# Performance work log

Measured on AMD Instinct MI355X. Metric: run time of the kernel, lower is better.

## Reference

```python
import jax, jax.numpy as jnp
import numpy as np

D_MODEL = 1024
EXPAND = 2
D_INNER = D_MODEL * EXPAND  # 2048
D_CONV = 4
B, T = 4, 4096
LN_EPS = 1e-5


def setup_inputs() -> dict:
    key = jax.random.key(0)
    ks = jax.random.split(key, 6)
    x = jax.random.normal(ks[0], (B, T, D_MODEL), dtype=jnp.float32)
    gamma = jnp.ones((D_MODEL,), jnp.float32)
    beta = jnp.zeros((D_MODEL,), jnp.float32)
    # in_proj: Linear(d_model -> 2*d_inner, bias=False); torch weight [out,in]
    W_in = jax.random.normal(ks[1], (2 * D_INNER, D_MODEL), jnp.float32) / np.sqrt(D_MODEL)
    # depthwise conv1d: weight [d_inner, 1, d_conv], bias [d_inner]
    conv_w = jax.random.normal(ks[2], (D_INNER, 1, D_CONV), jnp.float32) / np.sqrt(D_CONV)
    conv_b = jax.random.normal(ks[3], (D_INNER,), jnp.float32) * 0.01
    # out_proj: Linear(d_inner -> d_model, bias=False)
    W_out = jax.random.normal(ks[4], (D_MODEL, D_INNER), jnp.float32) / np.sqrt(D_INNER)
    return {"x": x, "gamma": gamma, "beta": beta, "W_in": W_in,
            "conv_w": conv_w, "conv_b": conv_b, "W_out": W_out}


def _silu(v):
    return v * jax.nn.sigmoid(v)


def reference(x, gamma, beta, W_in, conv_w, conv_b, W_out):
    residual = x
    # LayerNorm
    mu = jnp.mean(x, axis=-1, keepdims=True)
    var = jnp.mean(jnp.square(x - mu), axis=-1, keepdims=True)
    xn = (x - mu) * jax.lax.rsqrt(var + LN_EPS) * gamma + beta
    # in_proj -> split gate
    xz = jnp.einsum('btd,ed->bte', xn, W_in)  # [B,T,2*D_INNER]
    x_part, z = jnp.split(xz, 2, axis=-1)
    # causal depthwise conv: torch pads both sides by d_conv-1 then slices [:T]
    # == left pad (d_conv-1), no right pad
    lhs = jnp.transpose(x_part, (0, 2, 1))  # [B, D_INNER, T]
    x_conv = jax.lax.conv_general_dilated(
        lhs, conv_w, window_strides=(1,), padding=[(D_CONV - 1, 0)],
        feature_group_count=D_INNER,
        dimension_numbers=('NCH', 'OIH', 'NCH')) + conv_b[None, :, None]
    x_conv = jnp.transpose(x_conv, (0, 2, 1))  # [B,T,D_INNER]
    y = _silu(x_conv) * _silu(z)
    out = jnp.einsum('bte,de->btd', y, W_out)
    return residual + out  # dropout=0 (eval) -> identity
```

## Files before the change

### kernel.cpp

```cpp
#include <hip/hip_runtime.h>
#include <hip/hip_bf16.h>

#define D_MODEL 1024
#define D_INNER 2048
#define NTOK    16384
#define TLEN    4096
#define LN_EPS  1e-5f

typedef unsigned short u16;
typedef unsigned short u16x4 __attribute__((ext_vector_type(4)));
typedef unsigned short u16x8 __attribute__((ext_vector_type(8)));
typedef __bf16        bf16x8 __attribute__((ext_vector_type(8)));
typedef float         f32x4  __attribute__((ext_vector_type(4)));

__device__ __forceinline__ float b2f(u16 u) {
    union { float f; unsigned int i; } v; v.i = ((unsigned int)u) << 16; return v.f;
}
__device__ __forceinline__ u16 f2b(float f) {
    union { float f; unsigned int i; } v; v.f = f;
    unsigned int r = v.i + 0x7fffu + ((v.i >> 16) & 1u);
    return (u16)(r >> 16);
}

__device__ __forceinline__ void gld_lds16(const u16* g, u16* l) {
    __builtin_amdgcn_global_load_lds(
        (const __attribute__((address_space(1))) void*)g,
        (__attribute__((address_space(3))) void*)l, 16, 0, 0);
}

__device__ __forceinline__ void ln_body(
    int row, int tid,
    const float* __restrict__ x, const float* __restrict__ gamma,
    const float* __restrict__ beta, u16* __restrict__ xn)
{
    const float* xr = x + (size_t)row * D_MODEL;
    const int c0 = tid * 4;

    f32x4 xv = *(const f32x4*)(xr + c0);
    float s = 0.f, s2 = 0.f;
#pragma unroll
    for (int i = 0; i < 4; i++) { s += xv[i]; s2 += xv[i] * xv[i]; }

#pragma unroll
    for (int off = 32; off > 0; off >>= 1) {
        s  += __shfl_down(s,  off);
        s2 += __shfl_down(s2, off);
    }
    __shared__ float red[8];
    const int wave = tid >> 6, lane = tid & 63;
    if (lane == 0) { red[wave] = s; red[4 + wave] = s2; }
    __syncthreads();
    const float ts  = red[0] + red[1] + red[2] + red[3];
    const float ts2 = red[4] + red[5] + red[6] + red[7];
    const float mu  = ts * (1.0f / D_MODEL);
    const float var = ts2 * (1.0f / D_MODEL) - mu * mu;
    const float inv = rsqrtf(var + LN_EPS);

    f32x4 gv = *(const f32x4*)(gamma + c0);
    f32x4 bv = *(const f32x4*)(beta + c0);
    u16x4 out;
#pragma unroll
    for (int i = 0; i < 4; i++)
        out[i] = f2b((xv[i] - mu) * inv * gv[i] + bv[i]);
    *(u16x4*)(xn + (size_t)row * D_MODEL + c0) = out;
}

__global__ __launch_bounds__(256) void prep_kernel(
    const float* __restrict__ x, const float* __restrict__ gamma,
    const float* __restrict__ beta, u16* __restrict__ xn,
    const float* __restrict__ W_in, u16* __restrict__ wbin,
    const float* __restrict__ W_out, u16* __restrict__ wbout,
    const float* __restrict__ conv_w, float* __restrict__ wt,
    int lnRows)
{
    const int b   = blockIdx.x;
    const int tid = threadIdx.x;

    if (b < lnRows) {
        ln_body(b, tid, x, gamma, beta, xn);
        return;
    }
    int rb = b - lnRows;
    if (rb < 4096) {
        const int o = (rb * 256 + tid) * 4;
        f32x4 v = *(const f32x4*)(W_in + o);
        u16x4 w;
#pragma unroll
        for (int j = 0; j < 4; j++) w[j] = f2b(v[j]);
        *(u16x4*)(wbin + o) = w;
        return;
    }
    rb -= 4096;
    if (rb < 2048) {
        const int o = (rb * 256 + tid) * 4;
        f32x4 v = *(const f32x4*)(W_out + o);
        u16x4 w;
#pragma unroll
        for (int j = 0; j < 4; j++) w[j] = f2b(v[j]);
        *(u16x4*)(wbout + o) = w;
        return;
    }
    rb -= 2048;
    const int i = rb * 256 + tid;
    const int ch = i >> 2, j = i & 3;
    wt[j * D_INNER + ch] = conv_w[i];
}

__global__ __launch_bounds__(256) void ln_kernel(
    const float* __restrict__ x, const float* __restrict__ gamma,
    const float* __restrict__ beta, u16* __restrict__ xn)
{
    ln_body(blockIdx.x, threadIdx.x, x, gamma, beta, xn);
}

template<bool OUT_F32>
__global__ __launch_bounds__(256) void gemm_bt(
    const u16* __restrict__ A, const u16* __restrict__ Bt,
    void* __restrict__ Cv, const float* __restrict__ Res,
    int M, int N, int K)
{
    __shared__ u16 As[128 * 64];
    __shared__ u16 Bs[128 * 64];

    const int tid  = threadIdx.x;
    const int bm   = blockIdx.x;
    const int bn   = blockIdx.y;
    const int wave = tid >> 6;
    const int lane = tid & 63;
    const int wm = wave >> 1, wn = wave & 1;
    const int lane15 = lane & 15, quad = lane >> 4;

    f32x4 acc[4][4] = {};

    const u16* Ag = A  + (size_t)bm * 128 * K;
    const u16* Bg = Bt + (size_t)bn * 128 * K;

    const int lrow = lane >> 3;
    const int lcol = ((lane & 7) ^ lrow) * 8;

    const int sw = lane15 & 7;

    for (int kt = 0; kt < K; kt += 64) {
#pragma unroll
        for (int p = 0; p < 4; p++) {
            const int r = p * 32 + wave * 8;
            gld_lds16(Ag + (size_t)(r + lrow) * K + kt + lcol, &As[r * 64]);
            gld_lds16(Bg + (size_t)(r + lrow) * K + kt + lcol, &Bs[r * 64]);
        }
        __syncthreads();

#pragma unroll
        for (int kk = 0; kk < 64; kk += 32) {
            const int chunk = (((kk >> 3) + quad) ^ sw) * 8;
            bf16x8 af[4], bfr[4];
#pragma unroll
            for (int t = 0; t < 4; t++) {
                af[t]  = __builtin_bit_cast(bf16x8,
                    *(const u16x8*)(&As[(wm * 64 + t * 16 + lane15) * 64 + chunk]));
                bfr[t] = __builtin_bit_cast(bf16x8,
                    *(const u16x8*)(&Bs[(wn * 64 + t * 16 + lane15) * 64 + chunk]));
            }
#pragma unroll
            for (int tm = 0; tm < 4; tm++)
#pragma unroll
                for (int tn = 0; tn < 4; tn++)
                    acc[tm][tn] = __builtin_amdgcn_mfma_f32_16x16x32_bf16(
                        af[tm], bfr[tn], acc[tm][tn], 0, 0, 0);
        }
        __syncthreads();
    }

    const int m0 = bm * 128 + wm * 64 + quad * 4;
    const int n0 = bn * 128 + wn * 64 + lane15;
#pragma unroll
    for (int tm = 0; tm < 4; tm++) {
#pragma unroll
        for (int tn = 0; tn < 4; tn++) {
#pragma unroll
            for (int i = 0; i < 4; i++) {
                const int r  = m0 + tm * 16 + i;
                const int cc = n0 + tn * 16;
                const size_t idx = (size_t)r * N + cc;
                float v = acc[tm][tn][i];
                if (OUT_F32) {
                    ((float*)Cv)[idx] = v + Res[idx];
                } else {
                    ((u16*)Cv)[idx] = f2b(v);
                }
            }
        }
    }
}

__global__ __launch_bounds__(256) void conv_gate8(
    const u16* __restrict__ xz, const float* __restrict__ wt,
    const float* __restrict__ conv_b, u16* __restrict__ y)
{
    const int tid  = threadIdx.x;
    const int row0 = blockIdx.x * 8;
    const int c    = tid * 8;
    const int t0   = row0 & (TLEN - 1);

    float w[4][8];
#pragma unroll
    for (int j = 0; j < 4; j++) {
        f32x4 a = *(const f32x4*)(wt + j * D_INNER + c);
        f32x4 b = *(const f32x4*)(wt + j * D_INNER + c + 4);
#pragma unroll
        for (int u = 0; u < 4; u++) { w[j][u] = a[u]; w[j][4 + u] = b[u]; }
    }
    float bias[8];
    {
        f32x4 a = *(const f32x4*)(conv_b + c);
        f32x4 b = *(const f32x4*)(conv_b + c + 4);
#pragma unroll
        for (int u = 0; u < 4; u++) { bias[u] = a[u]; bias[4 + u] = b[u]; }
    }

    u16x8 xv[11];
    if (t0 != 0) {
#pragma unroll
        for (int k = 0; k < 3; k++)
            xv[k] = *(const u16x8*)(xz + (size_t)(row0 - 3 + k) * 4096 + c);
    } else {
#pragma unroll
        for (int k = 0; k < 3; k++) xv[k] = (u16x8)0;
    }
#pragma unroll
    for (int k = 3; k < 11; k++)
        xv[k] = *(const u16x8*)(xz + (size_t)(row0 - 3 + k) * 4096 + c);

#pragma unroll
    for (int i = 0; i < 8; i++) {
        float acc[8];
#pragma unroll
        for (int u = 0; u < 8; u++) acc[u] = bias[u];
#pragma unroll
        for (int j = 0; j < 4; j++)
#pragma unroll
            for (int u = 0; u < 8; u++)
                acc[u] += b2f(xv[i + j][u]) * w[j][u];

        u16x8 zv = *(const u16x8*)(xz + (size_t)(row0 + i) * 4096 + 2048 + c);
        u16x8 out;
#pragma unroll
        for (int u = 0; u < 8; u++) {
            const float a = acc[u];
            const float z = b2f(zv[u]);
            const float sa = a / (1.0f + __expf(-a));
            const float sz = z / (1.0f + __expf(-z));
            out[u] = f2b(sa * sz);
        }
        *(u16x8*)(y + (size_t)(row0 + i) * (size_t)D_INNER + c) = out;
    }
}

extern "C" void kernel_launch(void* const* d_in, const int* in_sizes, int n_in,
                              void* d_out, int out_size, void* d_ws, size_t ws_size,
                              hipStream_t stream)
{
    const float* x      = (const float*)d_in[0];
    const float* gamma  = (const float*)d_in[1];
    const float* beta   = (const float*)d_in[2];
    const float* W_in   = (const float*)d_in[3];
    const float* conv_w = (const float*)d_in[4];
    const float* conv_b = (const float*)d_in[5];
    const float* W_out  = (const float*)d_in[6];
    float* out = (float*)d_out;

    const int nWin  = 4096 * 1024;
    const int nWout = 1024 * 2048;
    const int nWc   = D_INNER * 4;

    u16*   wbin  = (u16*)d_ws;
    u16*   wbout = wbin + nWin;
    float* wt    = (float*)(wbout + nWout);
    u16*   base  = (u16*)(wt + nWc);

    const size_t wbytes = (size_t)(nWin + nWout) * sizeof(u16) + nWc * sizeof(float);
    const size_t perRow = (size_t)(D_MODEL + 4096 + D_INNER) * sizeof(u16);
    int NC = 4;
    if (ws_size >= wbytes + (size_t)NTOK * perRow)          NC = 1;
    else if (ws_size >= wbytes + (size_t)(NTOK/2) * perRow) NC = 2;
    const int RC = NTOK / NC;

    u16* xn = base;
    u16* xz = xn + (size_t)RC * D_MODEL;
    u16* y  = xz + (size_t)RC * 4096;

    const int lnRows = (NC == 1) ? NTOK : 0;
    prep_kernel<<<lnRows + 4096 + 2048 + 32, 256, 0, stream>>>(
        x, gamma, beta, xn, W_in, wbin, W_out, wbout, conv_w, wt, lnRows);

    for (int c = 0; c < NC; c++) {
        const float* xc   = x   + (size_t)c * RC * D_MODEL;
        float*       outc = out + (size_t)c * RC * D_MODEL;

        if (NC > 1)
            ln_kernel<<<RC, 256, 0, stream>>>(xc, gamma, beta, xn);

        dim3 g1(RC / 128, 4096 / 128);
        gemm_bt<false><<<g1, 256, 0, stream>>>(xn, wbin, xz, nullptr,
                                               RC, 2 * D_INNER, D_MODEL);

        conv_gate8<<<RC / 8, 256, 0, stream>>>(xz, wt, conv_b, y);

        dim3 g2(RC / 128, D_MODEL / 128);
        gemm_bt<true><<<g2, 256, 0, stream>>>(y, wbout, outc, xc,
                                              RC, D_MODEL, D_INNER);
    }
}
```

Before: 447.2 us.

## Replace 128x128 GEMM with double-buffered 256x256 pipelined MFMA kernel

Replaces the single-buffered 128x128 bf16 GEMM with a 256x256 tile, 512-thread kernel that double-buffers A/B in LDS and interleaves direct-to-LDS global loads with MFMA quarter-steps. It uses explicit vmcnt/lgkmcnt waits, barriers and s_setprio, and adds an XCD-aware block swizzle for L2 locality. The aim is to hide global load latency behind compute and raise arithmetic intensity per block. The cost is 128KB of LDS and heavy register use from 32 accumulators, and the hand-tuned wait counts are fragile to get right.

```diff
diff --git a/kernel.cpp b/kernel.cpp
--- a/kernel.cpp
+++ b/kernel.cpp
@@ -113,75 +113,157 @@
     ln_body(blockIdx.x, threadIdx.x, x, gamma, beta, xn);
 }
 
+#define BAR()      __builtin_amdgcn_s_barrier()
+#define LGKM0()    asm volatile("s_waitcnt lgkmcnt(0)" ::: "memory")
+#define WAIT_VM6() asm volatile("s_waitcnt vmcnt(6)" ::: "memory")
+#define WAIT_VM0() asm volatile("s_waitcnt vmcnt(0)" ::: "memory")
+
+#define STAGE_A(ldsb, s0, s1, kt) do { \
+    gld_lds16(Ag + (size_t)(s0) * K + (kt) + goff, &(ldsb)[(s0) * 64]); \
+    gld_lds16(Ag + (size_t)(s1) * K + (kt) + goff, &(ldsb)[(s1) * 64]); \
+} while (0)
+#define STAGE_B(ldsb, s0, s1, kt) do { \
+    gld_lds16(Bg + (size_t)(s0) * K + (kt) + goff, &(ldsb)[(s0) * 64]); \
+    gld_lds16(Bg + (size_t)(s1) * K + (kt) + goff, &(ldsb)[(s1) * 64]); \
+} while (0)
+
+#define RD_A(base, roff) do { \
+    _Pragma("unroll") for (int m_ = 0; m_ < 4; m_++) { \
+        const u16* p_ = (base) + (arow0 + (roff) + m_ * 16) * 64; \
+        aF[m_][0] = __builtin_bit_cast(bf16x8, *(const u16x8*)(p_ + cx0)); \
+        aF[m_][1] = __builtin_bit_cast(bf16x8, *(const u16x8*)(p_ + cx1)); \
+    } } while (0)
+#define RD_B(base, dst, roff) do { \
+    _Pragma("unroll") for (int n_ = 0; n_ < 2; n_++) { \
+        const u16* p_ = (base) + (brow0 + (roff) + n_ * 16) * 64; \
+        dst[n_][0] = __builtin_bit_cast(bf16x8, *(const u16x8*)(p_ + cx0)); \
+        dst[n_][1] = __builtin_bit_cast(bf16x8, *(const u16x8*)(p_ + cx1)); \
+    } } while (0)
+
+#define MMA_Q(m0, n0, BB) do { \
+    _Pragma("unroll") for (int m_ = 0; m_ < 4; m_++) \
+    _Pragma("unroll") for (int n_ = 0; n_ < 2; n_++) \
+    _Pragma("unroll") for (int k_ = 0; k_ < 2; k_++) \
+        acc[(m0) + m_][(n0) + n_] = __builtin_amdgcn_mfma_f32_16x16x32_bf16( \
+            aF[m_][k_], BB[n_][k_], acc[(m0) + m_][(n0) + n_], 0, 0, 0); \
+} while (0)
+
 template<bool OUT_F32>
-__global__ __launch_bounds__(256) void gemm_bt(
+__global__ __launch_bounds__(512, 2) void gemm256(
     const u16* __restrict__ A, const u16* __restrict__ Bt,
     void* __restrict__ Cv, const float* __restrict__ Res,
     int M, int N, int K)
 {
-    __shared__ u16 As[128 * 64];
-    __shared__ u16 Bs[128 * 64];
+    __shared__ u16 As[2][256 * 64];
+    __shared__ u16 Bs[2][256 * 64];
 
     const int tid  = threadIdx.x;
-    const int bm   = blockIdx.x;
-    const int bn   = blockIdx.y;
     const int wave = tid >> 6;
     const int lane = tid & 63;
-    const int wm = wave >> 1, wn = wave & 1;
+    const int wm = wave >> 2, wn = wave & 3;
     const int lane15 = lane & 15, quad = lane >> 4;
 
-    f32x4 acc[4][4] = {};
-
-    const u16* Ag = A  + (size_t)bm * 128 * K;
-    const u16* Bg = Bt + (size_t)bn * 128 * K;
+    const int gx   = gridDim.x;
+    const int nwg  = gx * gridDim.y;
+    const int flat = blockIdx.y * gx + blockIdx.x;
+    const int q8   = nwg >> 3;
+    const int swz  = (flat & 7) * q8 + (flat >> 3);
+    const int bm = swz % gx, bn = swz / gx;
+
+    const u16* Ag = A  + (size_t)bm * 256 * K;
+    const u16* Bg = Bt + (size_t)bn * 256 * K;
 
     const int lrow = lane >> 3;
     const int lcol = ((lane & 7) ^ lrow) * 8;
-
-    const int sw = lane15 & 7;
-
-    for (int kt = 0; kt < K; kt += 64) {
-#pragma unroll
-        for (int p = 0; p < 4; p++) {
-            const int r = p * 32 + wave * 8;
-            gld_lds16(Ag + (size_t)(r + lrow) * K + kt + lcol, &As[r * 64]);
-            gld_lds16(Bg + (size_t)(r + lrow) * K + kt + lcol, &Bs[r * 64]);
+    const size_t goff = (size_t)lrow * K + lcol;
+
+    const int aEv0 = wave * 8,      aEv1 = 128 + wave * 8;
+    const int aOd0 = 64 + wave * 8, aOd1 = 192 + wave * 8;
+    const int bEv0 = (wave >> 2) * 64 + (wave & 3) * 8, bEv1 = 128 + bEv0;
+    const int bOd0 = bEv0 + 32,     bOd1 = bEv1 + 32;
+
+    const int arow0 = wm * 128 + lane15;
+    const int brow0 = wn * 64  + lane15;
+    const int sw8   = lane15 & 7;
+    const int cx0   = ((quad ^ sw8) << 3);
+    const int cx1   = cx0 ^ 32;
+
+    f32x4  acc[8][4] = {};
+    bf16x8 aF[4][2], bE[2][2], bO[2][2];
+
+    const int NT = K >> 6;
+    const int NI = NT >> 1;
+
+    STAGE_A(As[0], aEv0, aEv1, 0);
+    STAGE_B(Bs[0], bEv0, bEv1, 0);
+    STAGE_B(Bs[0], bOd0, bOd1, 0);
+    STAGE_A(As[0], aOd0, aOd1, 0);
+    STAGE_A(As[1], aEv0, aEv1, 64);
+    STAGE_B(Bs[1], bEv0, bEv1, 64);
+    STAGE_B(Bs[1], bOd0, bOd1, 64);
+    WAIT_VM6();
+    BAR();
+
+    for (int i = 0; i < NI; i++) {
+        const int kt0   = i * 128;
+        const bool more = (i + 1 < NI);
+#pragma unroll
+        for (int h = 0; h < 2; h++) {
+            const u16* as = As[h];
+            const u16* bs = Bs[h];
+            const int ktA = kt0 + 64  + h * 64;
+            const int ktS = kt0 + 128 + h * 64;
+            const bool gA = (h == 0) || more;
+            const bool gS = more;
+
+            RD_A(as, 0);
+            RD_B(bs, bE, 0);
+            if (gA) STAGE_A(As[h ^ 1], aOd0, aOd1, ktA);
+            BAR(); LGKM0();
+            __builtin_amdgcn_s_setprio(1);
+            MMA_Q(0, 0, bE);
+            __builtin_amdgcn_s_setprio(0);
+            BAR();
+
+            RD_B(bs, bO, 32);
+            if (gS) STAGE_A(As[h], aEv0, aEv1, ktS);
+            BAR(); LGKM0();
+            __builtin_amdgcn_s_setprio(1);
+            MMA_Q(0, 2, bO);
+            __builtin_amdgcn_s_setprio(0);
+            BAR();
+
+            RD_A(as, 64);
+            if (gS) STAGE_B(Bs[h], bEv0, bEv1, ktS);
+            BAR(); LGKM0();
+            __builtin_amdgcn_s_setprio(1);
+            MMA_Q(4, 0, bE);
+            __builtin_amdgcn_s_setprio(0);
+            BAR();
+
+            if (gS) STAGE_B(Bs[h], bOd0, bOd1, ktS);
+            BAR(); LGKM0();
+            __builtin_amdgcn_s_setprio(1);
+            MMA_Q(4, 2, bO);
+            __builtin_amdgcn_s_setprio(0);
+            if (more)       WAIT_VM6();
+            else if (h == 0) WAIT_VM0();
+            BAR();
         }
-        __syncthreads();
-
-#pragma unroll
-        for (int kk = 0; kk < 64; kk += 32) {
-            const int chunk = (((kk >> 3) + quad) ^ sw) * 8;
-            bf16x8 af[4], bfr[4];
-#pragma unroll
-            for (int t = 0; t < 4; t++) {
-                af[t]  = __builtin_bit_cast(bf16x8,
-                    *(const u16x8*)(&As[(wm * 64 + t * 16 + lane15) * 64 + chunk]));
-                bfr[t] = __builtin_bit_cast(bf16x8,
-                    *(const u16x8*)(&Bs[(wn * 64 + t * 16 + lane15) * 64 + chunk]));
-            }
-#pragma unroll
-            for (int tm = 0; tm < 4; tm++)
-#pragma unroll
-                for (int tn = 0; tn < 4; tn++)
-                    acc[tm][tn] = __builtin_amdgcn_mfma_f32_16x16x32_bf16(
-                        af[tm], bfr[tn], acc[tm][tn], 0, 0, 0);
-        }
-        __syncthreads();
-    }
-
-    const int m0 = bm * 128 + wm * 64 + quad * 4;
-    const int n0 = bn * 128 + wn * 64 + lane15;
-#pragma unroll
-    for (int tm = 0; tm < 4; tm++) {
-#pragma unroll
-        for (int tn = 0; tn < 4; tn++) {
+    }
+
+    const int m0 = bm * 256 + wm * 128 + quad * 4;
+    const int n0 = bn * 256 + wn * 64 + lane15;
+#pragma unroll
+    for (int mf = 0; mf < 8; mf++) {
+#pragma unroll
+        for (int nf = 0; nf < 4; nf++) {
 #pragma unroll
             for (int i = 0; i < 4; i++) {
-                const int r  = m0 + tm * 16 + i;
-                const int cc = n0 + tn * 16;
+                const int r  = m0 + mf * 16 + i;
+                const int cc = n0 + nf * 16;
                 const size_t idx = (size_t)r * N + cc;
-                float v = acc[tm][tn][i];
+                float v = acc[mf][nf][i];
                 if (OUT_F32) {
                     ((float*)Cv)[idx] = v + Res[idx];
                 } else {
@@ -299,14 +381,14 @@
         if (NC > 1)
             ln_kernel<<<RC, 256, 0, stream>>>(xc, gamma, beta, xn);
 
-        dim3 g1(RC / 128, 4096 / 128);
-        gemm_bt<false><<<g1, 256, 0, stream>>>(xn, wbin, xz, nullptr,
+        dim3 g1(RC / 256, (2 * D_INNER) / 256);
+        gemm256<false><<<g1, 512, 0, stream>>>(xn, wbin, xz, nullptr,
                                                RC, 2 * D_INNER, D_MODEL);
 
         conv_gate8<<<RC / 8, 256, 0, stream>>>(xz, wt, conv_b, y);
 
-        dim3 g2(RC / 128, D_MODEL / 128);
-        gemm_bt<true><<<g2, 256, 0, stream>>>(y, wbout, outc, xc,
+        dim3 g2(RC / 256, D_MODEL / 256);
+        gemm256<true><<<g2, 512, 0, stream>>>(y, wbout, outc, xc,
                                               RC, D_MODEL, D_INNER);
     }
 }
```

New measurement: 405.3 us. 1.1x faster.
